# Performance work log

Hardware: AMD Instinct MI355X
Metric: run time of the kernel (lower is better)

## Reference

```python
import jax, jax.numpy as jnp
import numpy as np

N_NODES = 100000
N_EDGES = 1000000
HIDDEN = 64
NUM_CONVS = 3
EPS = 0.0  # GINEConv eps, not trained


def setup_inputs() -> dict:
    key = jax.random.key(0)
    ks = jax.random.split(key, 8)
    z = jax.random.randint(ks[0], (N_NODES,), 0, 100, dtype=jnp.int32)
    edge_index = jax.random.randint(ks[1], (2, N_EDGES), 0, N_NODES, dtype=jnp.int32)
    edge_attr = jax.random.normal(ks[2], (N_EDGES, HIDDEN), dtype=jnp.float32)
    node_emb = jax.random.normal(ks[3], (100, HIDDEN), dtype=jnp.float32)
    s = 1.0 / np.sqrt(HIDDEN)
    W1 = jax.random.uniform(ks[4], (NUM_CONVS, HIDDEN, HIDDEN), jnp.float32, -s, s)
    b1 = jax.random.uniform(ks[5], (NUM_CONVS, HIDDEN), jnp.float32, -s, s)
    W2 = jax.random.uniform(ks[6], (NUM_CONVS, HIDDEN, HIDDEN), jnp.float32, -s, s)
    b2 = jax.random.uniform(ks[7], (NUM_CONVS, HIDDEN), jnp.float32, -s, s)
    return {"node_emb": node_emb, "W1": W1, "b1": b1, "W2": W2, "b2": b2,
            "edge_attr": edge_attr, "z": z, "edge_index": edge_index}


def reference(node_emb, W1, b1, W2, b2, edge_attr, z, edge_index):
    x = node_emb[z]  # [N, H]
    src = edge_index[0]  # x_j (source, message sender)
    dst = edge_index[1]  # aggregation target i
    n = x.shape[0]
    for i in range(NUM_CONVS):
        # message: relu(x_j + edge_attr), scatter-add to target nodes
        msg = jax.nn.relu(x[src] + edge_attr)          # [E, H]
        agg = jax.ops.segment_sum(msg, dst, num_segments=n)  # [N, H]
        out = agg + (1.0 + EPS) * x
        # 2-layer MLP: Linear -> relu -> Linear (no act on last layer)
        h = jax.nn.relu(out @ W1[i].T + b1[i])
        h = h @ W2[i].T + b2[i]
        if i < NUM_CONVS - 1:
            h = jax.nn.relu(h)  # encoder-level activation between convs
        h = h + x  # short_cut residual
        x = h
    return x
```

## Files before the change

kernel.cpp:

```cpp
#include <hip/hip_runtime.h>

#define N_NODES 100000
#define N_EDGES 1000000
#define HID 64
#define SCAN_B 1024
#define SCAN_NB ((N_NODES + SCAN_B - 1) / SCAN_B)
#define GATHER_BLOCKS ((N_NODES * 16) / 256)
#define HIST_BLOCKS ((N_EDGES + 255) / 256)

__global__ __launch_bounds__(256) void prep_kernel(
    const float* __restrict__ node_emb, const int* __restrict__ z,
    float* __restrict__ x, const int* __restrict__ dst, int* __restrict__ offs)
{
    if (blockIdx.x < GATHER_BLOCKS) {
        int t = blockIdx.x * 256 + threadIdx.x;
        int n = t >> 4, c = t & 15;
        if (n >= N_NODES) return;
        int zi = z[n];
        float4 v = ((const float4*)(node_emb + (size_t)zi * HID))[c];
        ((float4*)(x + (size_t)n * HID))[c] = v;
    } else {
        int e = (blockIdx.x - GATHER_BLOCKS) * 256 + threadIdx.x;
        if (e < N_EDGES) atomicAdd(&offs[dst[e]], 1);
    }
}

__global__ __launch_bounds__(1024) void scan1_kernel(
    int* __restrict__ offs, int* __restrict__ bsum)
{
    __shared__ int wsum[16];
    int tid = threadIdx.x, lane = tid & 63, wid = tid >> 6;
    int i = blockIdx.x * SCAN_B + tid;
    int v = (i < N_NODES) ? offs[i] : 0;
    int s = v;
#pragma unroll
    for (int d = 1; d < 64; d <<= 1) {
        int t = __shfl_up(s, (unsigned)d, 64);
        if (lane >= d) s += t;
    }
    if (lane == 63) wsum[wid] = s;
    __syncthreads();
    if (wid == 0) {
        int w = (lane < 16) ? wsum[lane] : 0;
#pragma unroll
        for (int d = 1; d < 16; d <<= 1) {
            int t = __shfl_up(w, (unsigned)d, 64);
            if (lane >= d) w += t;
        }
        if (lane < 16) wsum[lane] = w;
    }
    __syncthreads();
    int woff = (wid == 0) ? 0 : wsum[wid - 1];
    if (i < N_NODES) offs[i] = woff + s - v;
    if (tid == 1023) bsum[blockIdx.x] = wsum[15];
}

__global__ __launch_bounds__(128) void scan2_kernel(int* __restrict__ bsum)
{
    __shared__ int ws[2];
    int tid = threadIdx.x, lane = tid & 63, wid = tid >> 6;
    int v = (tid < SCAN_NB) ? bsum[tid] : 0;
    int s = v;
#pragma unroll
    for (int d = 1; d < 64; d <<= 1) {
        int t = __shfl_up(s, (unsigned)d, 64);
        if (lane >= d) s += t;
    }
    if (lane == 63) ws[wid] = s;
    __syncthreads();
    int add = (wid == 1) ? ws[0] : 0;
    if (tid < SCAN_NB) bsum[tid] = add + s - v;
}

__global__ __launch_bounds__(1024) void scan3_kernel(
    int* __restrict__ offs, const int* __restrict__ bsum)
{
    int i = blockIdx.x * SCAN_B + threadIdx.x;
    if (i < N_NODES) {
        int v = offs[i] + bsum[blockIdx.x];
        atomicExch(&offs[i], v);
    }
}

__global__ __launch_bounds__(256) void fill_kernel(
    const int* __restrict__ src, const int* __restrict__ dst,
    int* __restrict__ offs, int2* __restrict__ eid2)
{
    int e = blockIdx.x * 256 + threadIdx.x;
    if (e < N_EDGES) {
        int d = dst[e];
        int pos = atomicAdd(&offs[d], 1);
        eid2[pos] = make_int2(e, src[e]);
    }
}

__global__ __launch_bounds__(256) void sort_kernel(
    const int* __restrict__ offs, int2* __restrict__ eid2)
{
    int gt = blockIdx.x * 256 + threadIdx.x;
    int n = gt >> 6;
    int lane = threadIdx.x & 63;
    if (n >= N_NODES) return;
    int start = (n == 0) ? 0 : offs[n - 1];
    int end = offs[n];
    int deg = end - start;
    if (deg <= 1 || deg > 64) return;
    int ke = 0x7fffffff, vs = 0;
    if (lane < deg) { int2 t = eid2[start + lane]; ke = t.x; vs = t.y; }
#pragma unroll
    for (int k = 2; k <= 64; k <<= 1) {
        for (int j = k >> 1; j > 0; j >>= 1) {
            int partner = lane ^ j;
            int ke2 = __shfl(ke, partner, 64);
            int vs2 = __shfl(vs, partner, 64);
            bool up = ((lane & k) == 0);
            bool takemin = ((lane < partner) == up);
            bool sw = takemin ? (ke2 < ke) : (ke2 > ke);
            if (sw) { ke = ke2; vs = vs2; }
        }
    }
    if (lane < deg) eid2[start + lane] = make_int2(ke, vs);
}

__global__ __launch_bounds__(256) void agg_kernel(
    const float* __restrict__ x, const float* __restrict__ ea,
    const int2* __restrict__ eid2, const int* __restrict__ offs,
    float* __restrict__ agg)
{
    int gt = blockIdx.x * 256 + threadIdx.x;
    int n = gt >> 6;
    if (n >= N_NODES) return;
    int lane = threadIdx.x & 63;
    int g = lane >> 4, c4 = lane & 15;
    int nu = __builtin_amdgcn_readfirstlane(n);
    int start = (nu == 0) ? 0 : offs[nu - 1];
    int end = offs[nu];
    int deg = end - start;
    int2 my = make_int2(0, 0);
    if (lane < deg) my = eid2[start + lane];
    float4 acc = make_float4(0.f, 0.f, 0.f, 0.f);
    int dmax = deg < 64 ? deg : 64;
    int iters = (dmax + 3) >> 2;
    for (int j = 0; j < iters; ++j) {
        int k = g + 4 * j;
        int eidx = __shfl(my.x, k, 64);
        int sidx = __shfl(my.y, k, 64);
        if (k < dmax) {
            float4 e4 = ((const float4*)(ea + (size_t)eidx * HID))[c4];
            float4 x4 = ((const float4*)(x + (size_t)sidx * HID))[c4];
            acc.x += fmaxf(x4.x + e4.x, 0.f);
            acc.y += fmaxf(x4.y + e4.y, 0.f);
            acc.z += fmaxf(x4.z + e4.z, 0.f);
            acc.w += fmaxf(x4.w + e4.w, 0.f);
        }
    }
    for (int i = start + 64 + g; i < end; i += 4) {
        int2 p = eid2[i];
        float4 e4 = ((const float4*)(ea + (size_t)p.x * HID))[c4];
        float4 x4 = ((const float4*)(x + (size_t)p.y * HID))[c4];
        acc.x += fmaxf(x4.x + e4.x, 0.f);
        acc.y += fmaxf(x4.y + e4.y, 0.f);
        acc.z += fmaxf(x4.z + e4.z, 0.f);
        acc.w += fmaxf(x4.w + e4.w, 0.f);
    }
    acc.x += __shfl_xor(acc.x, 16, 64);
    acc.y += __shfl_xor(acc.y, 16, 64);
    acc.z += __shfl_xor(acc.z, 16, 64);
    acc.w += __shfl_xor(acc.w, 16, 64);
    acc.x += __shfl_xor(acc.x, 32, 64);
    acc.y += __shfl_xor(acc.y, 32, 64);
    acc.z += __shfl_xor(acc.z, 32, 64);
    acc.w += __shfl_xor(acc.w, 32, 64);
    if (g == 0) ((float4*)(agg + (size_t)n * HID))[c4] = acc;
}

#define REP16(M) M(0) M(1) M(2) M(3) M(4) M(5) M(6) M(7) \
                 M(8) M(9) M(10) M(11) M(12) M(13) M(14) M(15)

__global__ __launch_bounds__(256, 2) void mlp_kernel(
    const float* __restrict__ agg,
    const float* __restrict__ W1, const float* __restrict__ b1,
    const float* __restrict__ W2, const float* __restrict__ b2,
    float* __restrict__ x, int last_relu)
{
    __shared__ float sW1[HID * HID];
    __shared__ float sW2T[HID * HID];
    __shared__ float sb1[HID];
    int tid = threadIdx.x;
    for (int idx = tid; idx < HID * HID; idx += 256) {
        sW1[idx] = W1[idx];
        int r = idx >> 6, col = idx & 63;
        sW2T[col * HID + r] = W2[idx];
    }
    if (tid < HID) sb1[tid] = b1[tid];
    __syncthreads();

    int n = blockIdx.x * 256 + tid;
    if (n >= N_NODES) return;

    const float4* ap = (const float4*)(agg + (size_t)n * HID);
    const float4* xp = (const float4*)(x + (size_t)n * HID);
    const float4* b2p = (const float4*)b2;

#define DECL_IN(k) float4 in##k; { float4 a = ap[k], b = xp[k]; \
    in##k.x = a.x + b.x; in##k.y = a.y + b.y; \
    in##k.z = a.z + b.z; in##k.w = a.w + b.w; }
    REP16(DECL_IN)
#undef DECL_IN

#define DECL_O(k) float4 o##k = b2p[k];
    REP16(DECL_O)
#undef DECL_O

    for (int j = 0; j < HID; ++j) {
        const float4* w1p = (const float4*)(sW1 + j * HID);
        float a0 = 0.f, a1 = 0.f, a2 = 0.f, a3 = 0.f;
#define DOT4(k, acc) { float4 w = w1p[k]; \
    acc += in##k.x * w.x + in##k.y * w.y + in##k.z * w.z + in##k.w * w.w; }
        DOT4(0, a0)  DOT4(1, a1)  DOT4(2, a2)  DOT4(3, a3)
        DOT4(4, a0)  DOT4(5, a1)  DOT4(6, a2)  DOT4(7, a3)
        DOT4(8, a0)  DOT4(9, a1)  DOT4(10, a2) DOT4(11, a3)
        DOT4(12, a0) DOT4(13, a1) DOT4(14, a2) DOT4(15, a3)
#undef DOT4
        float h = fmaxf((a0 + a1) + (a2 + a3) + sb1[j], 0.f);
        const float4* w2p = (const float4*)(sW2T + j * HID);
#define AXPY(k) { float4 w = w2p[k]; \
    o##k.x += h * w.x; o##k.y += h * w.y; \
    o##k.z += h * w.z; o##k.w += h * w.w; }
        REP16(AXPY)
#undef AXPY
    }

    float4* orow = (float4*)(x + (size_t)n * HID);
#define STORE(k) { float4 xv = xp[k]; float4 r; \
    r.x = (last_relu ? fmaxf(o##k.x, 0.f) : o##k.x) + xv.x; \
    r.y = (last_relu ? fmaxf(o##k.y, 0.f) : o##k.y) + xv.y; \
    r.z = (last_relu ? fmaxf(o##k.z, 0.f) : o##k.z) + xv.z; \
    r.w = (last_relu ? fmaxf(o##k.w, 0.f) : o##k.w) + xv.w; \
    orow[k] = r; }
    REP16(STORE)
#undef STORE
}

extern "C" void kernel_launch(void* const* d_in, const int* in_sizes, int n_in,
                              void* d_out, int out_size, void* d_ws, size_t ws_size,
                              hipStream_t stream) {
    const float* node_emb = (const float*)d_in[0];
    const float* W1 = (const float*)d_in[1];
    const float* b1 = (const float*)d_in[2];
    const float* W2 = (const float*)d_in[3];
    const float* b2 = (const float*)d_in[4];
    const float* ea = (const float*)d_in[5];
    const int* z = (const int*)d_in[6];
    const int* ei = (const int*)d_in[7];
    const int* src = ei;
    const int* dst = ei + N_EDGES;

    float* x = (float*)d_out;
    float* agg = (float*)d_ws;
    int2* eid2 = (int2*)(agg + (size_t)N_NODES * HID);
    int* offs = (int*)(eid2 + N_EDGES);
    int* bsum = offs + N_NODES;

    const int eb = (N_EDGES + 255) / 256;
    const int nodewave_blocks = (N_NODES * 64) / 256;
    const int mlp_blocks = (N_NODES + 255) / 256;

    hipMemsetAsync(offs, 0, N_NODES * sizeof(int), stream);
    prep_kernel<<<GATHER_BLOCKS + HIST_BLOCKS, 256, 0, stream>>>(
        node_emb, z, x, dst, offs);
    scan1_kernel<<<SCAN_NB, SCAN_B, 0, stream>>>(offs, bsum);
    scan2_kernel<<<1, 128, 0, stream>>>(bsum);
    scan3_kernel<<<SCAN_NB, SCAN_B, 0, stream>>>(offs, bsum);
    fill_kernel<<<eb, 256, 0, stream>>>(src, dst, offs, eid2);
    sort_kernel<<<nodewave_blocks, 256, 0, stream>>>(offs, eid2);

    for (int conv = 0; conv < 3; ++conv) {
        agg_kernel<<<nodewave_blocks, 256, 0, stream>>>(x, ea, eid2, offs, agg);
        mlp_kernel<<<mlp_blocks, 256, 0, stream>>>(
            agg, W1 + conv * HID * HID, b1 + conv * HID,
            W2 + conv * HID * HID, b2 + conv * HID,
            x, conv < 2 ? 1 : 0);
    }
}
```

Measured before the change: 942.6 us.

## Compute node MLP with bf16 MFMA matrix instructions instead of scalar FP32

Replaces the per-thread scalar FP32 two-layer MLP with per-wavefront 16-node tiles computed using bf16 16x16x32 MFMA instructions. Inputs and weights are converted to bf16 on the fly, and weights are loaded straight from global memory rather than staged in shared memory. The hidden activations pass through a small shared-memory buffer to change fragment layout between the two matmuls. This removes the FP32 FMA-bound loop and the weight staging, at the cost of bf16 rounding error in the MLP.

```diff
diff --git a/kernel.cpp b/kernel.cpp
--- a/kernel.cpp
+++ b/kernel.cpp
@@ -7,6 +7,27 @@
 #define SCAN_NB ((N_NODES + SCAN_B - 1) / SCAN_B)
 #define GATHER_BLOCKS ((N_NODES * 16) / 256)
 #define HIST_BLOCKS ((N_EDGES + 255) / 256)
+
+typedef __attribute__((ext_vector_type(8))) short short8;
+typedef __attribute__((ext_vector_type(4))) float f32x4;
+
+__device__ __forceinline__ unsigned short f2bf(float f) {
+    unsigned u = __float_as_uint(f);
+    u += 0x7fffu + ((u >> 16) & 1u);
+    return (unsigned short)(u >> 16);
+}
+__device__ __forceinline__ short8 pack8(float4 a, float4 b) {
+    short8 r;
+    r[0] = (short)f2bf(a.x); r[1] = (short)f2bf(a.y);
+    r[2] = (short)f2bf(a.z); r[3] = (short)f2bf(a.w);
+    r[4] = (short)f2bf(b.x); r[5] = (short)f2bf(b.y);
+    r[6] = (short)f2bf(b.z); r[7] = (short)f2bf(b.w);
+    return r;
+}
+__device__ __forceinline__ short8 ldw(const float* __restrict__ W, int row, int k0) {
+    const float4* p = (const float4*)(W + (size_t)row * HID + k0);
+    return pack8(p[0], p[1]);
+}
 
 __global__ __launch_bounds__(256) void prep_kernel(
     const float* __restrict__ node_emb, const int* __restrict__ z,
@@ -174,72 +195,73 @@
     if (g == 0) ((float4*)(agg + (size_t)n * HID))[c4] = acc;
 }
 
-#define REP16(M) M(0) M(1) M(2) M(3) M(4) M(5) M(6) M(7) \
-                 M(8) M(9) M(10) M(11) M(12) M(13) M(14) M(15)
-
-__global__ __launch_bounds__(256, 2) void mlp_kernel(
+__global__ __launch_bounds__(256) void mlp_kernel(
     const float* __restrict__ agg,
     const float* __restrict__ W1, const float* __restrict__ b1,
     const float* __restrict__ W2, const float* __restrict__ b2,
     float* __restrict__ x, int last_relu)
 {
-    __shared__ float sW1[HID * HID];
-    __shared__ float sW2T[HID * HID];
-    __shared__ float sb1[HID];
+    __shared__ unsigned short hl[4][16][64];
     int tid = threadIdx.x;
-    for (int idx = tid; idx < HID * HID; idx += 256) {
-        sW1[idx] = W1[idx];
-        int r = idx >> 6, col = idx & 63;
-        sW2T[col * HID + r] = W2[idx];
-    }
-    if (tid < HID) sb1[tid] = b1[tid];
-    __syncthreads();
-
-    int n = blockIdx.x * 256 + tid;
-    if (n >= N_NODES) return;
-
-    const float4* ap = (const float4*)(agg + (size_t)n * HID);
-    const float4* xp = (const float4*)(x + (size_t)n * HID);
-    const float4* b2p = (const float4*)b2;
-
-#define DECL_IN(k) float4 in##k; { float4 a = ap[k], b = xp[k]; \
-    in##k.x = a.x + b.x; in##k.y = a.y + b.y; \
-    in##k.z = a.z + b.z; in##k.w = a.w + b.w; }
-    REP16(DECL_IN)
-#undef DECL_IN
-
-#define DECL_O(k) float4 o##k = b2p[k];
-    REP16(DECL_O)
-#undef DECL_O
-
-    for (int j = 0; j < HID; ++j) {
-        const float4* w1p = (const float4*)(sW1 + j * HID);
-        float a0 = 0.f, a1 = 0.f, a2 = 0.f, a3 = 0.f;
-#define DOT4(k, acc) { float4 w = w1p[k]; \
-    acc += in##k.x * w.x + in##k.y * w.y + in##k.z * w.z + in##k.w * w.w; }
-        DOT4(0, a0)  DOT4(1, a1)  DOT4(2, a2)  DOT4(3, a3)
-        DOT4(4, a0)  DOT4(5, a1)  DOT4(6, a2)  DOT4(7, a3)
-        DOT4(8, a0)  DOT4(9, a1)  DOT4(10, a2) DOT4(11, a3)
-        DOT4(12, a0) DOT4(13, a1) DOT4(14, a2) DOT4(15, a3)
-#undef DOT4
-        float h = fmaxf((a0 + a1) + (a2 + a3) + sb1[j], 0.f);
-        const float4* w2p = (const float4*)(sW2T + j * HID);
-#define AXPY(k) { float4 w = w2p[k]; \
-    o##k.x += h * w.x; o##k.y += h * w.y; \
-    o##k.z += h * w.z; o##k.w += h * w.w; }
-        REP16(AXPY)
-#undef AXPY
-    }
-
-    float4* orow = (float4*)(x + (size_t)n * HID);
-#define STORE(k) { float4 xv = xp[k]; float4 r; \
-    r.x = (last_relu ? fmaxf(o##k.x, 0.f) : o##k.x) + xv.x; \
-    r.y = (last_relu ? fmaxf(o##k.y, 0.f) : o##k.y) + xv.y; \
-    r.z = (last_relu ? fmaxf(o##k.z, 0.f) : o##k.z) + xv.z; \
-    r.w = (last_relu ? fmaxf(o##k.w, 0.f) : o##k.w) + xv.w; \
-    orow[k] = r; }
-    REP16(STORE)
-#undef STORE
+    int wid = tid >> 6, lane = tid & 63;
+    int g = lane >> 4, c = lane & 15;
+    int m0 = (blockIdx.x * 4 + wid) * 16;
+    if (m0 >= N_NODES) return;
+
+    const float* arow = agg + (size_t)(m0 + c) * HID;
+    const float* xrow = x + (size_t)(m0 + c) * HID;
+    short8 af0, af1;
+    {
+        int k0 = g * 8;
+        float4 a0 = *(const float4*)(arow + k0), a1 = *(const float4*)(arow + k0 + 4);
+        float4 y0 = *(const float4*)(xrow + k0), y1 = *(const float4*)(xrow + k0 + 4);
+        af0 = pack8(make_float4(a0.x + y0.x, a0.y + y0.y, a0.z + y0.z, a0.w + y0.w),
+                    make_float4(a1.x + y1.x, a1.y + y1.y, a1.z + y1.z, a1.w + y1.w));
+        int k1 = 32 + g * 8;
+        float4 b0 = *(const float4*)(arow + k1), b1v = *(const float4*)(arow + k1 + 4);
+        float4 z0 = *(const float4*)(xrow + k1), z1 = *(const float4*)(xrow + k1 + 4);
+        af1 = pack8(make_float4(b0.x + z0.x, b0.y + z0.y, b0.z + z0.z, b0.w + z0.w),
+                    make_float4(b1v.x + z1.x, b1v.y + z1.y, b1v.z + z1.z, b1v.w + z1.w));
+    }
+
+    f32x4 a10 = {0.f, 0.f, 0.f, 0.f}, a11 = a10, a12 = a10, a13 = a10;
+#define L1(JT, ACC) { \
+    short8 w0 = ldw(W1, (JT)*16 + c, g * 8); \
+    short8 w1 = ldw(W1, (JT)*16 + c, 32 + g * 8); \
+    ACC = __builtin_amdgcn_mfma_f32_16x16x32_bf16(af0, w0, ACC, 0, 0, 0); \
+    ACC = __builtin_amdgcn_mfma_f32_16x16x32_bf16(af1, w1, ACC, 0, 0, 0); }
+    L1(0, a10) L1(1, a11) L1(2, a12) L1(3, a13)
+#undef L1
+
+#define HST(JT, ACC) { float bb = b1[(JT) * 16 + c]; \
+    hl[wid][4*g + 0][(JT)*16 + c] = f2bf(fmaxf(ACC[0] + bb, 0.f)); \
+    hl[wid][4*g + 1][(JT)*16 + c] = f2bf(fmaxf(ACC[1] + bb, 0.f)); \
+    hl[wid][4*g + 2][(JT)*16 + c] = f2bf(fmaxf(ACC[2] + bb, 0.f)); \
+    hl[wid][4*g + 3][(JT)*16 + c] = f2bf(fmaxf(ACC[3] + bb, 0.f)); }
+    HST(0, a10) HST(1, a11) HST(2, a12) HST(3, a13)
+#undef HST
+
+    short8 hf0 = *(const short8*)&hl[wid][c][g * 8];
+    short8 hf1 = *(const short8*)&hl[wid][c][32 + g * 8];
+
+    f32x4 a20 = {0.f, 0.f, 0.f, 0.f}, a21 = a20, a22 = a20, a23 = a20;
+#define L2(CT, ACC) { \
+    short8 w0 = ldw(W2, (CT)*16 + c, g * 8); \
+    short8 w1 = ldw(W2, (CT)*16 + c, 32 + g * 8); \
+    ACC = __builtin_amdgcn_mfma_f32_16x16x32_bf16(hf0, w0, ACC, 0, 0, 0); \
+    ACC = __builtin_amdgcn_mfma_f32_16x16x32_bf16(hf1, w1, ACC, 0, 0, 0); }
+    L2(0, a20) L2(1, a21) L2(2, a22) L2(3, a23)
+#undef L2
+
+#define EPI(CT, ACC) { float bb = b2[(CT) * 16 + c]; \
+    _Pragma("unroll") \
+    for (int r = 0; r < 4; ++r) { \
+        size_t idx = (size_t)(m0 + 4*g + r) * HID + (CT) * 16 + c; \
+        float o = ACC[r] + bb; \
+        if (last_relu) o = fmaxf(o, 0.f); \
+        x[idx] = o + x[idx]; } }
+    EPI(0, a20) EPI(1, a21) EPI(2, a22) EPI(3, a23)
+#undef EPI
 }
 
 extern "C" void kernel_launch(void* const* d_in, const int* in_sizes, int n_in,
@@ -264,7 +286,7 @@
 
     const int eb = (N_EDGES + 255) / 256;
     const int nodewave_blocks = (N_NODES * 64) / 256;
-    const int mlp_blocks = (N_NODES + 255) / 256;
+    const int mlp_blocks = (N_NODES / 16 + 3) / 4;
 
     hipMemsetAsync(offs, 0, N_NODES * sizeof(int), stream);
     prep_kernel<<<GATHER_BLOCKS + HIST_BLOCKS, 256, 0, stream>>>(
```

New measurement: 803.8 us. 14.7% less time.
